# Kernel tuning notes

Measured on AMD Instinct MI355X. Metric: run time of the kernel, lower is better.

The kernel has to match this reference:

```python
import jax, jax.numpy as jnp
import numpy as np
from jax import lax

N, L, C_IN, NOISE_C, COMP, NC = 256, 512, 514, 112, 16, 2
MAIN_IN = NOISE_C + COMP  # 128
FEAT = NC * 4 * L         # 4096

def _conv1d(x, w, b, pad):
    # x [N,C,L], w [O,I,K]
    y = lax.conv_general_dilated(x, w, (1,), [(pad, pad)], dimension_numbers=('NCH', 'OIH', 'NCH'))
    return y + b[None, :, None]

def _bn(x, g, b):
    # BatchNorm1d, training mode: biased batch stats over (N, L)
    m = x.mean(axis=(0, 2), keepdims=True)
    v = x.var(axis=(0, 2), keepdims=True)
    return (x - m) * lax.rsqrt(v + 1e-5) * g[None, :, None] + b[None, :, None]

def _lrelu(x):
    return jnp.where(x >= 0, x, 0.2 * x)

def _pos_encode(length, dim):
    j = np.arange(dim)
    div = 1.0 / np.power(10000.0, 2 * (j[:, None] // 2) / dim)   # [dim,1]
    ang = np.arange(length)[None, :] * div                       # [dim,length]
    ang = np.where((j % 2 == 0)[:, None], np.sin(ang), np.cos(ang))
    return jnp.asarray(ang[None], jnp.float32)                   # [1,dim,length]

def _assemble(circle_prob, slider_prob):
    # Vectorized run-length label expansion equivalent to the per-sample python while-loop.
    # circle_prob [N, L/2, 2], slider_prob [N, L/4, 2] -> [N, L, 3]
    n, B = slider_prob.shape[0], slider_prob.shape[1]
    c = jnp.argmax(circle_prob, -1)
    s = jnp.argmax(slider_prob, -1)
    zc = jnp.zeros(circle_prob.shape[:-1] + (1,), circle_prob.dtype)
    zs = jnp.zeros(slider_prob.shape[:-1] + (1,), slider_prob.dtype)
    cp3 = jnp.concatenate([circle_prob, zc], -1)                                   # insert 0 at class 2
    sp3 = jnp.concatenate([slider_prob[..., :1], zs, slider_prob[..., 1:]], -1)    # insert 0 at class 1
    pad100 = jnp.array([1., 0., 0.], cp3.dtype)
    pad001 = jnp.array([0., 0., 1.], cp3.dtype)
    bidx = jnp.arange(B)[None, :]
    # slider-body blocks: slider run continues and not cut by sequence end
    body = (s == 1) & (bidx < B - 1)
    prev_body = jnp.concatenate([jnp.zeros((n, 1), bool), body[:, :-1]], 1)
    # tail block ends a slider run (either run stops, or boundary block)
    tail = ((s == 1) & (bidx == B - 1)) | ((s == 0) & prev_body)
    # circle emission for each half-step: prob row if predicted circle else pad
    cr0 = jnp.where((c == 1)[..., None], cp3, pad100).reshape(n, B, 2, 3)
    bodyE = body[..., None]
    row0 = jnp.where((body | tail)[..., None], sp3, cr0[:, :, 0, :])
    row1 = jnp.where(bodyE, pad001, pad100)
    row2 = jnp.where(bodyE, pad001, cr0[:, :, 1, :])
    row3 = jnp.where(bodyE, pad001, pad100)
    return jnp.stack([row0, row1, row2, row3], 2).reshape(n, 4 * B, 3)

def _forward(noise, cond_data, gumbel_u, ext_w1, ext_b1, ext_w2, ext_b2, ext_bn_g, ext_bn_b,
             m_w1, m_b1, m_w2, m_b2, m_bn_g, m_bn_b, lin_w, lin_b, circ_w, circ_b, slid_w, slid_b):
    # FeatureExtractor
    x = cond_data.transpose(0, 2, 1)                      # [N, 514, L]
    x = _lrelu(_conv1d(x, ext_w1, ext_b1, 0))             # [N, 32, L]
    cond = _bn(_conv1d(x, ext_w2, ext_b2, 1), ext_bn_g, ext_bn_b)  # [N, 16, L]
    gen_in = jnp.concatenate([cond, noise.transpose(0, 2, 1)], 1) + _pos_encode(L, MAIN_IN)  # [N,128,L]
    h = _lrelu(_conv1d(gen_in, m_w1, m_b1, 3))            # [N, 32, L]
    h = _lrelu(_bn(_conv1d(h, m_w2, m_b2, 1), m_bn_g, m_bn_b))     # [N, 8, L]
    flat = _lrelu(h.reshape(h.shape[0], -1) @ lin_w + lin_b)       # [N, 4096]
    circle_prob = (flat @ circ_w + circ_b).reshape(-1, L // 2, NC)
    slider_prob = (flat @ slid_w + slid_b).reshape(-1, L // 4, NC)
    out = _assemble(circle_prob, slider_prob)             # [N, L, 3]
    # gumbel_softmax(hard=True, tau=1)
    g = -jnp.log(-jnp.log(gumbel_u + 1e-10) + 1e-10)
    logits = out + g
    y_soft = jax.nn.softmax(logits, -1)
    y_hard = jax.nn.one_hot(jnp.argmax(logits, -1), 3, dtype=y_soft.dtype)
    gen_out = y_hard + y_soft - lax.stop_gradient(y_soft)
    return gen_out, cond

def setup_inputs() -> dict:
    key = jax.random.key(0)
    ks = jax.random.split(key, 12)
    def rn(k, shape, fan_in):
        return jax.random.normal(k, shape, jnp.float32) * (1.0 / fan_in) ** 0.5
    return {
        'noise': jax.random.normal(ks[0], (N, L, NOISE_C), jnp.float32),
        'cond_data': jax.random.normal(ks[1], (N, L, C_IN), jnp.float32),
        'gumbel_u': jax.random.uniform(ks[2], (N, L, 3), jnp.float32),
        'ext_w1': rn(ks[3], (C_IN // 16, C_IN, 1), C_IN), 'ext_b1': jnp.zeros(C_IN // 16),
        'ext_w2': rn(ks[4], (COMP, C_IN // 16, 3), 3 * (C_IN // 16)), 'ext_b2': jnp.zeros(COMP),
        'ext_bn_g': jnp.ones(COMP), 'ext_bn_b': jnp.zeros(COMP),
        'm_w1': rn(ks[5], (NC * 16, MAIN_IN, 7), 7 * MAIN_IN), 'm_b1': jnp.zeros(NC * 16),
        'm_w2': rn(ks[6], (NC * 4, NC * 16, 3), 3 * NC * 16), 'm_b2': jnp.zeros(NC * 4),
        'm_bn_g': jnp.ones(NC * 4), 'm_bn_b': jnp.zeros(NC * 4),
        'lin_w': rn(ks[7], (FEAT, FEAT), FEAT), 'lin_b': jnp.zeros(FEAT),
        'circ_w': rn(ks[8], (FEAT, NC * L // 2), FEAT), 'circ_b': jnp.zeros(NC * L // 2),
        'slid_w': rn(ks[9], (FEAT, NC * L // 4), FEAT), 'slid_b': jnp.zeros(NC * L // 4),
    }

def reference(noise, cond_data, gumbel_u, ext_w1, ext_b1, ext_w2, ext_b2, ext_bn_g, ext_bn_b,
              m_w1, m_b1, m_w2, m_b2, m_bn_g, m_bn_b, lin_w, lin_b, circ_w, circ_b, slid_w, slid_b):
    return _forward(noise, cond_data, gumbel_u, ext_w1, ext_b1, ext_w2, ext_b2, ext_bn_g, ext_bn_b,
                    m_w1, m_b1, m_w2, m_b2, m_bn_g, m_bn_b, lin_w, lin_b, circ_w, circ_b, slid_w, slid_b)
```

## Files before the change

### kernel.cpp

```cpp
#include <hip/hip_runtime.h>
#include <math.h>

#define NB 256
#define LL 512
#define CIN 514

__device__ __forceinline__ float lrelu(float x) { return x >= 0.f ? x : 0.2f * x; }

__global__ __launch_bounds__(256) void k_pos(float* __restrict__ pos) {
    int idx = blockIdx.x * 256 + threadIdx.x;
    int c = idx >> 9, l = idx & 511;
    double e = (double)(2 * (c >> 1)) / 128.0;
    double dv = 1.0 / pow(10000.0, e);
    double a = (double)l * dv;
    pos[idx] = (float)((c & 1) ? cos(a) : sin(a));
}

__global__ __launch_bounds__(256) void k_posconv(const float* __restrict__ POS, const float* __restrict__ W,
                                                 const float* __restrict__ bias, float* __restrict__ PC) {
    const int t = threadIdx.x;
    const int o = blockIdx.x >> 4, l0 = (blockIdx.x & 15) * 32;
    const int l = l0 + (t & 31), cs = t >> 5;
    float acc = 0.f;
    for (int ci = 0; ci < 16; ++ci) {
        int c = cs * 16 + ci;
        float wv[7];
#pragma unroll
        for (int k = 0; k < 7; ++k) wv[k] = W[o * 896 + c * 7 + k];
#pragma unroll
        for (int k = 0; k < 7; ++k) {
            int gl = l + k - 3;
            if (gl >= 0 && gl < LL) acc += wv[k] * POS[c * LL + gl];
        }
    }
    __shared__ float red[8][33];
    red[cs][t & 31] = acc;
    __syncthreads();
    if (cs == 0) {
        float s = bias[o];
#pragma unroll
        for (int j = 0; j < 8; ++j) s += red[j][t & 31];
        PC[o * LL + l0 + (t & 31)] = s;
    }
}

__global__ __launch_bounds__(256) void k_conv1(const float* __restrict__ X, const float* __restrict__ W,
                                               float* __restrict__ Pbase) {
    __shared__ __align__(16) float As[16][524];
    __shared__ __align__(16) float Bs[16][36];
    const int t = threadIdx.x;
    const int n = blockIdx.x >> 2, z = blockIdx.x & 3;
    const int kbase = z * 128;
    const int nch = (z == 3) ? 9 : 8;
    const int tl = t & 63, to = t >> 6;
    const size_t rowbase = (size_t)n * 512 * CIN;

    float acc[8][8];
#pragma unroll
    for (int oi = 0; oi < 8; ++oi)
#pragma unroll
        for (int p = 0; p < 8; ++p) acc[oi][p] = 0.f;

    float2 pf[16];
    float2 pfb;

    {
        const int kb = kbase;
#pragma unroll
        for (int ps = 0; ps < 16; ++ps) {
            int idx = ps * 256 + t;
            int pos = idx >> 3, kp = idx & 7;
            int gk = kb + kp * 2;
            float2 v = {0.f, 0.f};
            if (gk + 1 < CIN) v = *(const float2*)(X + rowbase + (size_t)pos * CIN + gk);
            else if (gk < CIN) v.x = X[rowbase + (size_t)pos * CIN + gk];
            pf[ps] = v;
        }
        {
            int o = t >> 3, kp = t & 7;
            int gk = kb + kp * 2;
            float2 v = {0.f, 0.f};
            if (gk + 1 < CIN) v = *(const float2*)(W + (size_t)o * CIN + gk);
            else if (gk < CIN) v.x = W[(size_t)o * CIN + gk];
            pfb = v;
        }
#pragma unroll
        for (int ps = 0; ps < 16; ++ps) {
            int idx = ps * 256 + t;
            int pos = idx >> 3, kp = idx & 7;
            As[kp * 2][pos] = pf[ps].x;
            As[kp * 2 + 1][pos] = pf[ps].y;
        }
        {
            int o = t >> 3, kp = t & 7;
            Bs[kp * 2][o] = pfb.x;
            Bs[kp * 2 + 1][o] = pfb.y;
        }
    }
    __syncthreads();

    for (int c = 0; c < nch; ++c) {
        if (c + 1 < nch) {
            const int kb = kbase + (c + 1) * 16;
#pragma unroll
            for (int ps = 0; ps < 16; ++ps) {
                int idx = ps * 256 + t;
                int pos = idx >> 3, kp = idx & 7;
                int gk = kb + kp * 2;
                float2 v = {0.f, 0.f};
                if (gk + 1 < CIN) v = *(const float2*)(X + rowbase + (size_t)pos * CIN + gk);
                else if (gk < CIN) v.x = X[rowbase + (size_t)pos * CIN + gk];
                pf[ps] = v;
            }
            int o = t >> 3, kp = t & 7;
            int gk = kb + kp * 2;
            float2 v = {0.f, 0.f};
            if (gk + 1 < CIN) v = *(const float2*)(W + (size_t)o * CIN + gk);
            else if (gk < CIN) v.x = W[(size_t)o * CIN + gk];
            pfb = v;
        }
#pragma unroll
        for (int kk = 0; kk < 16; ++kk) {
            float4 aL = *(const float4*)&As[kk][tl * 4];
            float4 aH = *(const float4*)&As[kk][256 + tl * 4];
            float4 b0 = *(const float4*)&Bs[kk][to * 8];
            float4 b1 = *(const float4*)&Bs[kk][to * 8 + 4];
            float av[8] = {aL.x, aL.y, aL.z, aL.w, aH.x, aH.y, aH.z, aH.w};
            float bv[8] = {b0.x, b0.y, b0.z, b0.w, b1.x, b1.y, b1.z, b1.w};
#pragma unroll
            for (int oi = 0; oi < 8; ++oi)
#pragma unroll
                for (int p = 0; p < 8; ++p) acc[oi][p] += av[p] * bv[oi];
        }
        __syncthreads();
        if (c + 1 < nch) {
#pragma unroll
            for (int ps = 0; ps < 16; ++ps) {
                int idx = ps * 256 + t;
                int pos = idx >> 3, kp = idx & 7;
                As[kp * 2][pos] = pf[ps].x;
                As[kp * 2 + 1][pos] = pf[ps].y;
            }
            int o = t >> 3, kp = t & 7;
            Bs[kp * 2][o] = pfb.x;
            Bs[kp * 2 + 1][o] = pfb.y;
        }
        __syncthreads();
    }

    float* P = Pbase + (size_t)z * 4194304;
#pragma unroll
    for (int oi = 0; oi < 8; ++oi) {
        int o = to * 8 + oi;
        float4 v0 = {acc[oi][0], acc[oi][1], acc[oi][2], acc[oi][3]};
        float4 v1 = {acc[oi][4], acc[oi][5], acc[oi][6], acc[oi][7]};
        *(float4*)(P + ((size_t)n * 32 + o) * LL + tl * 4) = v0;
        *(float4*)(P + ((size_t)n * 32 + o) * LL + 256 + tl * 4) = v1;
    }
}

__global__ __launch_bounds__(256) void k_conv2(const float* __restrict__ Pbase,
                                               const float* __restrict__ b1, const float* __restrict__ W,
                                               const float* __restrict__ bias, float* __restrict__ out) {
    __shared__ __align__(16) float Xs[32][264];
    __shared__ __align__(16) float Ws[16][32][4];
    const int t = threadIdx.x;
    const int n = blockIdx.x >> 1, l0 = (blockIdx.x & 1) * 256;
    for (int idx = t; idx < 32 * 258; idx += 256) {
        int i = idx / 258, j = idx % 258;
        int gl = l0 - 1 + j;
        float v = 0.f;
        if (gl >= 0 && gl < LL) {
            size_t off = ((size_t)n * 32 + i) * LL + gl;
            v = lrelu(Pbase[off] + Pbase[off + 4194304] + Pbase[off + 8388608] + Pbase[off + 12582912] + b1[i]);
        }
        Xs[i][j] = v;
    }
    for (int idx = t; idx < 1536; idx += 256) {
        int o = idx / 96, r = idx % 96;
        Ws[o][r / 3][r % 3] = W[idx];
    }
    __syncthreads();
    const int tx = t & 31, ty = t >> 5;
    float acc[2][8];
#pragma unroll
    for (int q = 0; q < 2; ++q)
#pragma unroll
        for (int p = 0; p < 8; ++p) acc[q][p] = 0.f;
    for (int i = 0; i < 32; ++i) {
        float4 a0 = *(const float4*)&Xs[i][tx*8];
        float4 a1 = *(const float4*)&Xs[i][tx*8+4];
        float4 a2 = *(const float4*)&Xs[i][tx*8+8];
        float a[12] = {a0.x,a0.y,a0.z,a0.w,a1.x,a1.y,a1.z,a1.w,a2.x,a2.y,a2.z,a2.w};
#pragma unroll
        for (int q = 0; q < 2; ++q) {
            float4 b = *(const float4*)&Ws[ty*2+q][i][0];
#pragma unroll
            for (int p = 0; p < 8; ++p)
                acc[q][p] += a[p]*b.x + a[p+1]*b.y + a[p+2]*b.z;
        }
    }
#pragma unroll
    for (int q = 0; q < 2; ++q) {
        int o = ty*2+q; float bb = bias[o];
#pragma unroll
        for (int h = 0; h < 2; ++h) {
            float4 v;
            v.x = acc[q][h*4+0] + bb; v.y = acc[q][h*4+1] + bb;
            v.z = acc[q][h*4+2] + bb; v.w = acc[q][h*4+3] + bb;
            *(float4*)(out + ((size_t)n*16 + o)*LL + l0 + tx*8 + h*4) = v;
        }
    }
}

__global__ __launch_bounds__(256) void k_redstats(const float* __restrict__ src, int C, float* __restrict__ part) {
    const int ch = blockIdx.x, sl = blockIdx.y, t = threadIdx.x;
    float s = 0.f, q = 0.f;
    for (int i = t; i < 4096; i += 256) {
        int n = sl*8 + (i >> 9), l = i & 511;
        float v = src[((size_t)n*C + ch)*LL + l];
        s += v; q += v*v;
    }
    __shared__ float rs[256], rq[256];
    rs[t] = s; rq[t] = q;
    __syncthreads();
    for (int off = 128; off > 0; off >>= 1) {
        if (t < off) { rs[t] += rs[t+off]; rq[t] += rq[t+off]; }
        __syncthreads();
    }
    if (t == 0) { part[(ch*32+sl)*2] = rs[0]; part[(ch*32+sl)*2+1] = rq[0]; }
}

__global__ void k_bnfinal(const float* __restrict__ part, const float* __restrict__ g,
                          const float* __restrict__ b, int C, float* __restrict__ ss) {
    int ch = threadIdx.x;
    if (ch >= C) return;
    float s = 0.f, q = 0.f;
    for (int j = 0; j < 32; ++j) { s += part[(ch*32 + j)*2]; q += part[(ch*32 + j)*2 + 1]; }
    float mean = s * (1.f/131072.f);
    float var = q * (1.f/131072.f) - mean*mean;
    float sc = g[ch] / sqrtf(var + 1e-5f);
    ss[ch] = sc;
    ss[C + ch] = b[ch] - mean * sc;
}

__global__ __launch_bounds__(256) void k_bnapply(const float* __restrict__ src, const float* __restrict__ ss,
        int C, float* __restrict__ dst, int act, int total4) {
    int i4 = blockIdx.x * 256 + threadIdx.x;
    if (i4 >= total4) return;
    int i = i4 << 2;
    int ch = (i >> 9) % C;
    float sc = ss[ch], sh = ss[C + ch];
    float4 v = reinterpret_cast<const float4*>(src)[i4];
    v.x = v.x*sc + sh; v.y = v.y*sc + sh; v.z = v.z*sc + sh; v.w = v.w*sc + sh;
    if (act) { v.x = lrelu(v.x); v.y = lrelu(v.y); v.z = lrelu(v.z); v.w = lrelu(v.w); }
    reinterpret_cast<float4*>(dst)[i4] = v;
}

__global__ __launch_bounds__(256) void k_mconv1(const float* __restrict__ C16, const float* __restrict__ NZ,
        const float* __restrict__ PC, const float* __restrict__ W,
        float* __restrict__ out0, float* __restrict__ out1) {
    __shared__ __align__(16) float Gs[2][8][268];
    __shared__ __align__(16) float Ws[2][32][8][8];
    const int t = threadIdx.x;
    const int n = blockIdx.x >> 2, l0 = ((blockIdx.x >> 1) & 1) * 256, z = blockIdx.x & 1;
    const int tx = t & 31, ty = t >> 5;
    float acc[4][8];
#pragma unroll
    for (int q = 0; q < 4; ++q)
#pragma unroll
        for (int p = 0; p < 8; ++p) acc[q][p] = 0.f;

    float4 ga0, ga1, gb0, gb1;
    float wpf[8];
    const int gl1 = l0 - 3 + t;
    const bool ok1 = (gl1 >= 0 && gl1 < LL);
    const int gl2 = l0 + 253 + t;
    const bool ok2 = (t < 6) && (gl2 < LL);

    auto LOADG = [&](int hh) {
        const float4 f4z = {0.f, 0.f, 0.f, 0.f};
        ga0 = f4z; ga1 = f4z; gb0 = f4z; gb1 = f4z;
        if (z == 0 && hh < 2) {
            const float* base = C16 + ((size_t)n * 16 + hh * 8) * LL;
            if (ok1) {
                const float* p = base + gl1;
                ga0.x = p[0];      ga0.y = p[LL];     ga0.z = p[2*LL];  ga0.w = p[3*LL];
                ga1.x = p[4*LL];   ga1.y = p[5*LL];   ga1.z = p[6*LL];  ga1.w = p[7*LL];
            }
            if (ok2) {
                const float* p = base + gl2;
                gb0.x = p[0];      gb0.y = p[LL];     gb0.z = p[2*LL];  gb0.w = p[3*LL];
                gb1.x = p[4*LL];   gb1.y = p[5*LL];   gb1.z = p[6*LL];  gb1.w = p[7*LL];
            }
        } else {
            const int nzc = z * 64 + hh * 8 - 16;
            if (ok1) {
                const float* p = NZ + ((size_t)n * LL + gl1) * 112 + nzc;
                ga0 = *(const float4*)p;
                ga1 = *(const float4*)(p + 4);
            }
            if (ok2) {
                const float* p = NZ + ((size_t)n * LL + gl2) * 112 + nzc;
                gb0 = *(const float4*)p;
                gb1 = *(const float4*)(p + 4);
            }
        }
    };
    auto WRITEG = [&](int bb) {
        Gs[bb][0][t] = ga0.x; Gs[bb][1][t] = ga0.y; Gs[bb][2][t] = ga0.z; Gs[bb][3][t] = ga0.w;
        Gs[bb][4][t] = ga1.x; Gs[bb][5][t] = ga1.y; Gs[bb][6][t] = ga1.z; Gs[bb][7][t] = ga1.w;
        if (t < 6) {
            Gs[bb][0][256+t] = gb0.x; Gs[bb][1][256+t] = gb0.y; Gs[bb][2][256+t] = gb0.z; Gs[bb][3][256+t] = gb0.w;
            Gs[bb][4][256+t] = gb1.x; Gs[bb][5][256+t] = gb1.y; Gs[bb][6][256+t] = gb1.z; Gs[bb][7][256+t] = gb1.w;
        }
    };
    auto LOADW = [&](int hh) {
        const int b7 = (z * 64 + hh * 8) * 7;
#pragma unroll
        for (int p = 0; p < 8; ++p) {
            int idx = p * 256 + t;
            int k = idx & 7, ci = (idx >> 3) & 7, o = idx >> 6;
            wpf[p] = (k < 7) ? W[(size_t)o * 896 + b7 + ci * 7 + k] : 0.f;
        }
    };
    auto WRITEW = [&](int bb) {
#pragma unroll
        for (int p = 0; p < 8; ++p) {
            int idx = p * 256 + t;
            int k = idx & 7;
            if (k < 7) {
                int ci = (idx >> 3) & 7, o = idx >> 6;
                Ws[bb][o][ci][k] = wpf[p];
            }
        }
    };

    LOADG(0);
    LOADW(0);
    WRITEG(0);
    WRITEW(0);
    __syncthreads();

    for (int h = 0; h < 8; ++h) {
        const int hb = h & 1;
        if (h < 7) {
            LOADG(h + 1);
            LOADW(h + 1);
        }
        for (int ci = 0; ci < 8; ++ci) {
            float4 a0 = *(const float4*)&Gs[hb][ci][tx*4];
            float4 a1 = *(const float4*)&Gs[hb][ci][tx*4+4];
            float4 a2 = *(const float4*)&Gs[hb][ci][tx*4+8];
            float4 a3 = *(const float4*)&Gs[hb][ci][128+tx*4];
            float4 a4 = *(const float4*)&Gs[hb][ci][128+tx*4+4];
            float4 a5 = *(const float4*)&Gs[hb][ci][128+tx*4+8];
            float aA[12] = {a0.x,a0.y,a0.z,a0.w,a1.x,a1.y,a1.z,a1.w,a2.x,a2.y,a2.z,a2.w};
            float aB[12] = {a3.x,a3.y,a3.z,a3.w,a4.x,a4.y,a4.z,a4.w,a5.x,a5.y,a5.z,a5.w};
#pragma unroll
            for (int q = 0; q < 4; ++q) {
                float4 b0 = *(const float4*)&Ws[hb][ty*4+q][ci][0];
                float4 b1 = *(const float4*)&Ws[hb][ty*4+q][ci][4];
                float b[7] = {b0.x,b0.y,b0.z,b0.w,b1.x,b1.y,b1.z};
#pragma unroll
                for (int p = 0; p < 4; ++p) {
#pragma unroll
                    for (int k = 0; k < 7; ++k) {
                        acc[q][p]   += aA[p+k]*b[k];
                        acc[q][4+p] += aB[p+k]*b[k];
                    }
                }
            }
        }
        if (h < 7) {
            const int nb = hb ^ 1;
            WRITEG(nb);
            WRITEW(nb);
            __syncthreads();
        }
    }

    float* out = z ? out1 : out0;
#pragma unroll
    for (int q = 0; q < 4; ++q) {
        int o = ty*4 + q;
        float4 p0 = {0.f,0.f,0.f,0.f}, p1 = {0.f,0.f,0.f,0.f};
        if (z == 0) {
            p0 = *(const float4*)(PC + o*LL + l0 + tx*4);
            p1 = *(const float4*)(PC + o*LL + l0 + 128 + tx*4);
        }
        float4 v0 = {acc[q][0]+p0.x, acc[q][1]+p0.y, acc[q][2]+p0.z, acc[q][3]+p0.w};
        float4 v1 = {acc[q][4]+p1.x, acc[q][5]+p1.y, acc[q][6]+p1.z, acc[q][7]+p1.w};
        *(float4*)(out + ((size_t)n*32 + o)*LL + l0 + tx*4) = v0;
        *(float4*)(out + ((size_t)n*32 + o)*LL + l0 + 128 + tx*4) = v1;
    }
}

__global__ __launch_bounds__(256) void k_mconv2(const float* __restrict__ P0, const float* __restrict__ P1,
        const float* __restrict__ W, const float* __restrict__ bias, float* __restrict__ out) {
    __shared__ __align__(16) float Xs[32][264];
    __shared__ __align__(16) float Ws[8][32][4];
    const int t = threadIdx.x;
    const int n = blockIdx.x >> 1, l0 = (blockIdx.x & 1) * 256;
    for (int idx = t; idx < 32 * 258; idx += 256) {
        int i = idx / 258, j = idx % 258;
        int gl = l0 - 1 + j;
        float v = 0.f;
        if (gl >= 0 && gl < LL) {
            size_t off = ((size_t)n * 32 + i) * LL + gl;
            v = lrelu(P0[off] + P1[off]);
        }
        Xs[i][j] = v;
    }
    for (int idx = t; idx < 768; idx += 256) {
        int o = idx / 96, r = idx % 96;
        Ws[o][r / 3][r % 3] = W[idx];
    }
    __syncthreads();
    const int tx = t & 31, ty = t >> 5;
    float acc[8];
#pragma unroll
    for (int p = 0; p < 8; ++p) acc[p] = 0.f;
    for (int i = 0; i < 32; ++i) {
        float4 a0 = *(const float4*)&Xs[i][tx*8];
        float4 a1 = *(const float4*)&Xs[i][tx*8+4];
        float4 a2 = *(const float4*)&Xs[i][tx*8+8];
        float a[12] = {a0.x,a0.y,a0.z,a0.w,a1.x,a1.y,a1.z,a1.w,a2.x,a2.y,a2.z,a2.w};
        float4 b = *(const float4*)&Ws[ty][i][0];
#pragma unroll
        for (int p = 0; p < 8; ++p)
            acc[p] += a[p]*b.x + a[p+1]*b.y + a[p+2]*b.z;
    }
    float bb = bias[ty];
#pragma unroll
    for (int h = 0; h < 2; ++h) {
        float4 v;
        v.x = acc[h*4+0] + bb; v.y = acc[h*4+1] + bb;
        v.z = acc[h*4+2] + bb; v.w = acc[h*4+3] + bb;
        *(float4*)(out + ((size_t)n*8 + ty)*LL + l0 + tx*8 + h*4) = v;
    }
}

__global__ __launch_bounds__(256) void k_lin(const float* __restrict__ A, const float* __restrict__ B,
                                             float* __restrict__ part) {
    __shared__ __align__(16) float As[16][132];
    __shared__ __align__(16) float Bs[16][132];
    const int t = threadIdx.x;
    const int bid = blockIdx.x;
    const int xcd = bid & 7, j = bid >> 3;
    const int z = j >> 3;
    const int m0 = ((j >> 2) & 1) * 128;
    const int f0 = (xcd * 4 + (j & 3)) * 128;
    const int k0base = z * 256;
    const int sar = t & 127, saq = t >> 7;
    const int sbr = t >> 4, sbq = t & 15;
    const int mq = (t & 15) * 4, fq = (t >> 4) * 4;

    float acc[8][8];
#pragma unroll
    for (int i = 0; i < 8; ++i)
#pragma unroll
        for (int q = 0; q < 8; ++q) acc[i][q] = 0.f;

    for (int it = 0; it < 16; ++it) {
        const int k0 = k0base + it * 16;
        {
            const float* pA = A + (size_t)(m0 + sar) * 4096 + k0 + saq * 8;
            float4 a0 = *(const float4*)(pA);
            float4 a1 = *(const float4*)(pA + 4);
            const float* pB = B + (size_t)(k0 + sbr) * 4096 + f0 + sbq * 8;
            float4 b0 = *(const float4*)(pB);
            float4 b1 = *(const float4*)(pB + 4);
            As[saq*8+0][sar] = a0.x; As[saq*8+1][sar] = a0.y; As[saq*8+2][sar] = a0.z; As[saq*8+3][sar] = a0.w;
            As[saq*8+4][sar] = a1.x; As[saq*8+5][sar] = a1.y; As[saq*8+6][sar] = a1.z; As[saq*8+7][sar] = a1.w;
            *(float4*)&Bs[sbr][sbq*8] = b0;
            *(float4*)&Bs[sbr][sbq*8+4] = b1;
        }
        __syncthreads();
#pragma unroll
        for (int kk = 0; kk < 16; ++kk) {
            float4 a0 = *(const float4*)&As[kk][mq];
            float4 a1 = *(const float4*)&As[kk][mq + 64];
            float4 b0 = *(const float4*)&Bs[kk][fq];
            float4 b1 = *(const float4*)&Bs[kk][fq + 64];
            float av[8] = {a0.x,a0.y,a0.z,a0.w,a1.x,a1.y,a1.z,a1.w};
            float bv[8] = {b0.x,b0.y,b0.z,b0.w,b1.x,b1.y,b1.z,b1.w};
#pragma unroll
            for (int i = 0; i < 8; ++i)
#pragma unroll
                for (int q = 0; q < 8; ++q) acc[i][q] += av[i] * bv[q];
        }
        __syncthreads();
    }

#pragma unroll
    for (int i = 0; i < 8; ++i) {
        int m = m0 + mq + (i & 3) + (i >> 2) * 64;
        float4 v0 = {acc[i][0], acc[i][1], acc[i][2], acc[i][3]};
        float4 v1 = {acc[i][4], acc[i][5], acc[i][6], acc[i][7]};
        *(float4*)(part + ((size_t)z * 256 + m) * 4096 + f0 + fq) = v0;
        *(float4*)(part + ((size_t)z * 256 + m) * 4096 + f0 + fq + 64) = v1;
    }
}

__global__ __launch_bounds__(256) void k_linred(const float* __restrict__ part, const float* __restrict__ bias,
        float* __restrict__ out) {
    int i4 = blockIdx.x*256 + threadIdx.x;
    int i = i4 << 2;
    int f = i & 4095;
    float4 s = *(const float4*)(bias + f);
#pragma unroll
    for (int zz = 0; zz < 16; ++zz) {
        float4 p = ((const float4*)(part + (size_t)zz * 1048576))[i4];
        s.x += p.x; s.y += p.y; s.z += p.z; s.w += p.w;
    }
    float4 r;
    r.x = lrelu(s.x); r.y = lrelu(s.y); r.z = lrelu(s.z); r.w = lrelu(s.w);
    ((float4*)out)[i4] = r;
}

__global__ __launch_bounds__(256) void k_heads(const float* __restrict__ A, const float* __restrict__ CW,
        const float* __restrict__ SW, float* __restrict__ part) {
    __shared__ __align__(16) float As[32][36];
    __shared__ __align__(16) float Bs[32][132];
    const int t = threadIdx.x;
    const int m0 = blockIdx.x * 32, f0 = blockIdx.y * 128, z = blockIdx.z;
    const float* B; int ldb, fb;
    if (f0 < 512) { B = CW; ldb = 512; fb = f0; } else { B = SW; ldb = 256; fb = f0 - 512; }
    const int tm = t & 7, tf = t >> 3;
    const int mi = t >> 3, kq = t & 7;
    float acc[4][4];
#pragma unroll
    for (int pm = 0; pm < 4; ++pm)
#pragma unroll
        for (int pf = 0; pf < 4; ++pf) acc[pm][pf] = 0.f;
    for (int k0 = z * 256; k0 < z * 256 + 256; k0 += 32) {
        float4 av = *(const float4*)(A + (size_t)(m0 + mi) * 4096 + k0 + kq * 4);
        As[kq*4+0][mi] = av.x; As[kq*4+1][mi] = av.y; As[kq*4+2][mi] = av.z; As[kq*4+3][mi] = av.w;
#pragma unroll
        for (int pass = 0; pass < 4; ++pass) {
            int fi = pass * 32 + kq * 4;
            *(float4*)&Bs[mi][fi] = *(const float4*)(B + (size_t)(k0 + mi) * ldb + fb + fi);
        }
        __syncthreads();
#pragma unroll 8
        for (int kk = 0; kk < 32; ++kk) {
            float4 a = *(const float4*)&As[kk][tm * 4];
            float4 b = *(const float4*)&Bs[kk][tf * 4];
            float avv[4] = {a.x,a.y,a.z,a.w};
            float bvv[4] = {b.x,b.y,b.z,b.w};
#pragma unroll
            for (int pm = 0; pm < 4; ++pm)
#pragma unroll
                for (int pf = 0; pf < 4; ++pf) acc[pm][pf] += avv[pm]*bvv[pf];
        }
        __syncthreads();
    }
#pragma unroll
    for (int pm = 0; pm < 4; ++pm) {
        float4 v = {acc[pm][0], acc[pm][1], acc[pm][2], acc[pm][3]};
        *(float4*)(part + ((size_t)z * 256 + m0 + tm * 4 + pm) * 768 + f0 + tf * 4) = v;
    }
}

__global__ __launch_bounds__(256) void k_assemble(const float* __restrict__ part, const float* __restrict__ cb,
        const float* __restrict__ sb, const float* __restrict__ gum, float* __restrict__ out) {
    __shared__ float buf[768];
    const int n = blockIdx.x;
    const int t = threadIdx.x;
#pragma unroll
    for (int rep = 0; rep < 3; ++rep) {
        int f = rep * 256 + t;
        float s = 0.f;
#pragma unroll
        for (int ks = 0; ks < 16; ++ks) s += part[((size_t)(ks * 256 + n)) * 768 + f];
        s += (f < 512) ? cb[f] : sb[f - 512];
        buf[f] = s;
    }
    __syncthreads();
    if (t >= 128) return;
    const int b = t;
    const float* cp = buf;
    const float* sp = buf + 512;
    float sl0 = sp[2*b], sl1 = sp[2*b+1];
    int s = sl1 > sl0 ? 1 : 0;
    int prevb = 0;
    if (b > 0) prevb = (sp[2*b-1] > sp[2*b-2]) ? 1 : 0;
    bool body = (s == 1) && (b < 127);
    bool tail = ((s == 1) && (b == 127)) || ((s == 0) && (prevb == 1));
    float c0a = cp[4*b], c0b = cp[4*b+1], c1a = cp[4*b+2], c1b = cp[4*b+3];
    bool cA = c0b > c0a, cB = c1b > c1a;
    float rows[4][3];
    if (body || tail)      { rows[0][0]=sl0; rows[0][1]=0.f; rows[0][2]=sl1; }
    else if (cA)           { rows[0][0]=c0a; rows[0][1]=c0b; rows[0][2]=0.f; }
    else                   { rows[0][0]=1.f; rows[0][1]=0.f; rows[0][2]=0.f; }
    if (body)              { rows[1][0]=0.f; rows[1][1]=0.f; rows[1][2]=1.f; }
    else                   { rows[1][0]=1.f; rows[1][1]=0.f; rows[1][2]=0.f; }
    if (body)              { rows[2][0]=0.f; rows[2][1]=0.f; rows[2][2]=1.f; }
    else if (cB)           { rows[2][0]=c1a; rows[2][1]=c1b; rows[2][2]=0.f; }
    else                   { rows[2][0]=1.f; rows[2][1]=0.f; rows[2][2]=0.f; }
    rows[3][0]=rows[1][0]; rows[3][1]=rows[1][1]; rows[3][2]=rows[1][2];
#pragma unroll
    for (int r = 0; r < 4; ++r) {
        int l = 4*b + r;
        const float* u = gum + ((size_t)n*512 + l)*3;
        float g0 = -logf(-logf(u[0]+1e-10f)+1e-10f);
        float g1 = -logf(-logf(u[1]+1e-10f)+1e-10f);
        float g2 = -logf(-logf(u[2]+1e-10f)+1e-10f);
        float t0 = rows[r][0]+g0, t1 = rows[r][1]+g1, t2 = rows[r][2]+g2;
        int am = 0; float mv = t0;
        if (t1 > mv) { am = 1; mv = t1; }
        if (t2 > mv) { am = 2; mv = t2; }
        float e0 = expf(t0-mv), e1 = expf(t1-mv), e2 = expf(t2-mv);
        float ssum = e0+e1+e2;
        float y0 = e0/ssum, y1 = e1/ssum, y2 = e2/ssum;
        float* o = out + ((size_t)n*512 + l)*3;
        o[0] = ((am==0?1.f:0.f) + y0) - y0;
        o[1] = ((am==1?1.f:0.f) + y1) - y1;
        o[2] = ((am==2?1.f:0.f) + y2) - y2;
    }
}

extern "C" void kernel_launch(void* const* d_in, const int* in_sizes, int n_in,
                              void* d_out, int out_size, void* d_ws, size_t ws_size,
                              hipStream_t stream) {
    const float* noise   = (const float*)d_in[0];
    const float* cond    = (const float*)d_in[1];
    const float* gumbel  = (const float*)d_in[2];
    const float* ext_w1  = (const float*)d_in[3];
    const float* ext_b1  = (const float*)d_in[4];
    const float* ext_w2  = (const float*)d_in[5];
    const float* ext_b2  = (const float*)d_in[6];
    const float* ext_bng = (const float*)d_in[7];
    const float* ext_bnb = (const float*)d_in[8];
    const float* m_w1    = (const float*)d_in[9];
    const float* m_b1    = (const float*)d_in[10];
    const float* m_w2    = (const float*)d_in[11];
    const float* m_b2    = (const float*)d_in[12];
    const float* m_bng   = (const float*)d_in[13];
    const float* m_bnb   = (const float*)d_in[14];
    const float* lin_w   = (const float*)d_in[15];
    const float* lin_b   = (const float*)d_in[16];
    const float* circ_w  = (const float*)d_in[17];
    const float* circ_b  = (const float*)d_in[18];
    const float* slid_w  = (const float*)d_in[19];
    const float* slid_b  = (const float*)d_in[20];

    float* genout  = (float*)d_out;
    float* condout = (float*)d_out + 256*512*3;

    float* w     = (float*)d_ws;
    float* ws0   = w;
    float* y2    = ws0 + 16777216;
    float* posb  = y2 + 2097152;
    float* pc    = posb + 65536;
    float* flatB = pc + 16384;
    float* partH = flatB + 1048576;
    float* stats = partH + 3145728;

    k_pos<<<256, 256, 0, stream>>>(posb);
    k_posconv<<<512, 256, 0, stream>>>(posb, m_w1, m_b1, pc);
    k_conv1<<<1024, 256, 0, stream>>>(cond, ext_w1, ws0);
    k_conv2<<<512, 256, 0, stream>>>(ws0, ext_b1, ext_w2, ext_b2, y2);
    k_redstats<<<dim3(16,32), 256, 0, stream>>>(y2, 16, stats);
    k_bnfinal<<<1, 64, 0, stream>>>(stats, ext_bng, ext_bnb, 16, stats + 2048);
    k_bnapply<<<2048, 256, 0, stream>>>(y2, stats + 2048, 16, condout, 0, 524288);
    k_mconv1<<<1024, 256, 0, stream>>>(condout, noise, pc, m_w1, ws0, ws0 + 4194304);
    k_mconv2<<<512, 256, 0, stream>>>(ws0, ws0 + 4194304, m_w2, m_b2, y2);
    k_redstats<<<dim3(8,32), 256, 0, stream>>>(y2, 8, stats);
    k_bnfinal<<<1, 64, 0, stream>>>(stats, m_bng, m_bnb, 8, stats + 2048 + 64);
    k_bnapply<<<1024, 256, 0, stream>>>(y2, stats + 2048 + 64, 8, y2, 1, 262144);
    k_lin<<<1024, 256, 0, stream>>>(y2, lin_w, ws0);
    k_linred<<<1024, 256, 0, stream>>>(ws0, lin_b, flatB);
    k_heads<<<dim3(8,6,16), 256, 0, stream>>>(flatB, circ_w, slid_w, partH);
    k_assemble<<<256, 256, 0, stream>>>(partH, circ_b, slid_b, gumbel, genout);
}
```

Baseline: 526.9 us.

## Fuse BN stat reduction into conv epilogues and register-prefetch GEMM tiles

Removes the separate k_redstats passes by computing per-block sum and sum-of-squares in the k_conv2 and k_mconv2 epilogues and writing 512 partials per channel, which k_bnfinal now reduces. The k_lin and k_heads loops now load the next K tile into registers while the current shared-memory tile is being consumed, so global load latency can overlap with the FMAs. The cost is an extra barrier per iteration, more register pressure in the GEMMs, and a longer serial loop in the single-block bnfinal kernel.

```diff
diff --git a/kernel.cpp b/kernel.cpp
--- a/kernel.cpp
+++ b/kernel.cpp
@@ -161,11 +161,14 @@
 
 __global__ __launch_bounds__(256) void k_conv2(const float* __restrict__ Pbase,
                                                const float* __restrict__ b1, const float* __restrict__ W,
-                                               const float* __restrict__ bias, float* __restrict__ out) {
+                                               const float* __restrict__ bias, float* __restrict__ out,
+                                               float* __restrict__ part) {
     __shared__ __align__(16) float Xs[32][264];
     __shared__ __align__(16) float Ws[16][32][4];
+    __shared__ float reds[16][33], redq[16][33];
     const int t = threadIdx.x;
-    const int n = blockIdx.x >> 1, l0 = (blockIdx.x & 1) * 256;
+    const int bid = blockIdx.x;
+    const int n = bid >> 1, l0 = (bid & 1) * 256;
     for (int idx = t; idx < 32 * 258; idx += 256) {
         int i = idx / 258, j = idx % 258;
         int gl = l0 - 1 + j;
@@ -203,40 +206,35 @@
 #pragma unroll
     for (int q = 0; q < 2; ++q) {
         int o = ty*2+q; float bb = bias[o];
+        float s = 0.f, sq = 0.f;
 #pragma unroll
         for (int h = 0; h < 2; ++h) {
             float4 v;
             v.x = acc[q][h*4+0] + bb; v.y = acc[q][h*4+1] + bb;
             v.z = acc[q][h*4+2] + bb; v.w = acc[q][h*4+3] + bb;
+            s += v.x + v.y + v.z + v.w;
+            sq += v.x*v.x + v.y*v.y + v.z*v.z + v.w*v.w;
             *(float4*)(out + ((size_t)n*16 + o)*LL + l0 + tx*8 + h*4) = v;
         }
-    }
-}
-
-__global__ __launch_bounds__(256) void k_redstats(const float* __restrict__ src, int C, float* __restrict__ part) {
-    const int ch = blockIdx.x, sl = blockIdx.y, t = threadIdx.x;
-    float s = 0.f, q = 0.f;
-    for (int i = t; i < 4096; i += 256) {
-        int n = sl*8 + (i >> 9), l = i & 511;
-        float v = src[((size_t)n*C + ch)*LL + l];
-        s += v; q += v*v;
-    }
-    __shared__ float rs[256], rq[256];
-    rs[t] = s; rq[t] = q;
-    __syncthreads();
-    for (int off = 128; off > 0; off >>= 1) {
-        if (t < off) { rs[t] += rs[t+off]; rq[t] += rq[t+off]; }
-        __syncthreads();
-    }
-    if (t == 0) { part[(ch*32+sl)*2] = rs[0]; part[(ch*32+sl)*2+1] = rq[0]; }
+        reds[o][tx] = s;
+        redq[o][tx] = sq;
+    }
+    __syncthreads();
+    if (t < 16) {
+        float s = 0.f, sq = 0.f;
+#pragma unroll
+        for (int x = 0; x < 32; ++x) { s += reds[t][x]; sq += redq[t][x]; }
+        part[((size_t)t * 512 + bid) * 2] = s;
+        part[((size_t)t * 512 + bid) * 2 + 1] = sq;
+    }
 }
 
 __global__ void k_bnfinal(const float* __restrict__ part, const float* __restrict__ g,
-                          const float* __restrict__ b, int C, float* __restrict__ ss) {
+                          const float* __restrict__ b, int C, int S, float* __restrict__ ss) {
     int ch = threadIdx.x;
     if (ch >= C) return;
     float s = 0.f, q = 0.f;
-    for (int j = 0; j < 32; ++j) { s += part[(ch*32 + j)*2]; q += part[(ch*32 + j)*2 + 1]; }
+    for (int j = 0; j < S; ++j) { s += part[((size_t)ch*S + j)*2]; q += part[((size_t)ch*S + j)*2 + 1]; }
     float mean = s * (1.f/131072.f);
     float var = q * (1.f/131072.f) - mean*mean;
     float sc = g[ch] / sqrtf(var + 1e-5f);
@@ -397,11 +395,14 @@
 }
 
 __global__ __launch_bounds__(256) void k_mconv2(const float* __restrict__ P0, const float* __restrict__ P1,
-        const float* __restrict__ W, const float* __restrict__ bias, float* __restrict__ out) {
+        const float* __restrict__ W, const float* __restrict__ bias, float* __restrict__ out,
+        float* __restrict__ part) {
     __shared__ __align__(16) float Xs[32][264];
     __shared__ __align__(16) float Ws[8][32][4];
+    __shared__ float reds[8][33], redq[8][33];
     const int t = threadIdx.x;
-    const int n = blockIdx.x >> 1, l0 = (blockIdx.x & 1) * 256;
+    const int bid = blockIdx.x;
+    const int n = bid >> 1, l0 = (bid & 1) * 256;
     for (int idx = t; idx < 32 * 258; idx += 256) {
         int i = idx / 258, j = idx % 258;
         int gl = l0 - 1 + j;
@@ -432,12 +433,25 @@
             acc[p] += a[p]*b.x + a[p+1]*b.y + a[p+2]*b.z;
     }
     float bb = bias[ty];
+    float s = 0.f, sq = 0.f;
 #pragma unroll
     for (int h = 0; h < 2; ++h) {
         float4 v;
         v.x = acc[h*4+0] + bb; v.y = acc[h*4+1] + bb;
         v.z = acc[h*4+2] + bb; v.w = acc[h*4+3] + bb;
+        s += v.x + v.y + v.z + v.w;
+        sq += v.x*v.x + v.y*v.y + v.z*v.z + v.w*v.w;
         *(float4*)(out + ((size_t)n*8 + ty)*LL + l0 + tx*8 + h*4) = v;
+    }
+    reds[ty][tx] = s;
+    redq[ty][tx] = sq;
+    __syncthreads();
+    if (t < 8) {
+        float ss = 0.f, qq = 0.f;
+#pragma unroll
+        for (int x = 0; x < 32; ++x) { ss += reds[t][x]; qq += redq[t][x]; }
+        part[((size_t)t * 512 + bid) * 2] = ss;
+        part[((size_t)t * 512 + bid) * 2 + 1] = qq;
     }
 }
 
@@ -462,21 +476,32 @@
 #pragma unroll
         for (int q = 0; q < 8; ++q) acc[i][q] = 0.f;
 
+    float4 pa0, pa1, pb0, pb1;
+    {
+        const int k0 = k0base;
+        const float* pA = A + (size_t)(m0 + sar) * 4096 + k0 + saq * 8;
+        pa0 = *(const float4*)(pA);
+        pa1 = *(const float4*)(pA + 4);
+        const float* pB = B + (size_t)(k0 + sbr) * 4096 + f0 + sbq * 8;
+        pb0 = *(const float4*)(pB);
+        pb1 = *(const float4*)(pB + 4);
+        As[saq*8+0][sar] = pa0.x; As[saq*8+1][sar] = pa0.y; As[saq*8+2][sar] = pa0.z; As[saq*8+3][sar] = pa0.w;
+        As[saq*8+4][sar] = pa1.x; As[saq*8+5][sar] = pa1.y; As[saq*8+6][sar] = pa1.z; As[saq*8+7][sar] = pa1.w;
+        *(float4*)&Bs[sbr][sbq*8] = pb0;
+        *(float4*)&Bs[sbr][sbq*8+4] = pb1;
+    }
+    __syncthreads();
+
     for (int it = 0; it < 16; ++it) {
-        const int k0 = k0base + it * 16;
-        {
+        if (it + 1 < 16) {
+            const int k0 = k0base + (it + 1) * 16;
             const float* pA = A + (size_t)(m0 + sar) * 4096 + k0 + saq * 8;
-            float4 a0 = *(const float4*)(pA);
-            float4 a1 = *(const float4*)(pA + 4);
+            pa0 = *(const float4*)(pA);
+            pa1 = *(const float4*)(pA + 4);
             const float* pB = B + (size_t)(k0 + sbr) * 4096 + f0 + sbq * 8;
-            float4 b0 = *(const float4*)(pB);
-            float4 b1 = *(const float4*)(pB + 4);
-            As[saq*8+0][sar] = a0.x; As[saq*8+1][sar] = a0.y; As[saq*8+2][sar] = a0.z; As[saq*8+3][sar] = a0.w;
-            As[saq*8+4][sar] = a1.x; As[saq*8+5][sar] = a1.y; As[saq*8+6][sar] = a1.z; As[saq*8+7][sar] = a1.w;
-            *(float4*)&Bs[sbr][sbq*8] = b0;
-            *(float4*)&Bs[sbr][sbq*8+4] = b1;
-        }
-        __syncthreads();
+            pb0 = *(const float4*)(pB);
+            pb1 = *(const float4*)(pB + 4);
+        }
 #pragma unroll
         for (int kk = 0; kk < 16; ++kk) {
             float4 a0 = *(const float4*)&As[kk][mq];
@@ -489,6 +514,13 @@
             for (int i = 0; i < 8; ++i)
 #pragma unroll
                 for (int q = 0; q < 8; ++q) acc[i][q] += av[i] * bv[q];
+        }
+        __syncthreads();
+        if (it + 1 < 16) {
+            As[saq*8+0][sar] = pa0.x; As[saq*8+1][sar] = pa0.y; As[saq*8+2][sar] = pa0.z; As[saq*8+3][sar] = pa0.w;
+            As[saq*8+4][sar] = pa1.x; As[saq*8+5][sar] = pa1.y; As[saq*8+6][sar] = pa1.z; As[saq*8+7][sar] = pa1.w;
+            *(float4*)&Bs[sbr][sbq*8] = pb0;
+            *(float4*)&Bs[sbr][sbq*8+4] = pb1;
         }
         __syncthreads();
     }
@@ -534,15 +566,29 @@
     for (int pm = 0; pm < 4; ++pm)
 #pragma unroll
         for (int pf = 0; pf < 4; ++pf) acc[pm][pf] = 0.f;
-    for (int k0 = z * 256; k0 < z * 256 + 256; k0 += 32) {
-        float4 av = *(const float4*)(A + (size_t)(m0 + mi) * 4096 + k0 + kq * 4);
-        As[kq*4+0][mi] = av.x; As[kq*4+1][mi] = av.y; As[kq*4+2][mi] = av.z; As[kq*4+3][mi] = av.w;
-#pragma unroll
-        for (int pass = 0; pass < 4; ++pass) {
-            int fi = pass * 32 + kq * 4;
-            *(float4*)&Bs[mi][fi] = *(const float4*)(B + (size_t)(k0 + mi) * ldb + fb + fi);
-        }
-        __syncthreads();
+
+    float4 pav, pbv[4];
+    {
+        const int k0 = z * 256;
+        pav = *(const float4*)(A + (size_t)(m0 + mi) * 4096 + k0 + kq * 4);
+#pragma unroll
+        for (int pass = 0; pass < 4; ++pass)
+            pbv[pass] = *(const float4*)(B + (size_t)(k0 + mi) * ldb + fb + pass * 32 + kq * 4);
+        As[kq*4+0][mi] = pav.x; As[kq*4+1][mi] = pav.y; As[kq*4+2][mi] = pav.z; As[kq*4+3][mi] = pav.w;
+#pragma unroll
+        for (int pass = 0; pass < 4; ++pass)
+            *(float4*)&Bs[mi][pass * 32 + kq * 4] = pbv[pass];
+    }
+    __syncthreads();
+
+    for (int it = 0; it < 8; ++it) {
+        if (it + 1 < 8) {
+            const int k0 = z * 256 + (it + 1) * 32;
+            pav = *(const float4*)(A + (size_t)(m0 + mi) * 4096 + k0 + kq * 4);
+#pragma unroll
+            for (int pass = 0; pass < 4; ++pass)
+                pbv[pass] = *(const float4*)(B + (size_t)(k0 + mi) * ldb + fb + pass * 32 + kq * 4);
+        }
 #pragma unroll 8
         for (int kk = 0; kk < 32; ++kk) {
             float4 a = *(const float4*)&As[kk][tm * 4];
@@ -553,6 +599,13 @@
             for (int pm = 0; pm < 4; ++pm)
 #pragma unroll
                 for (int pf = 0; pf < 4; ++pf) acc[pm][pf] += avv[pm]*bvv[pf];
+        }
+        __syncthreads();
+        if (it + 1 < 8) {
+            As[kq*4+0][mi] = pav.x; As[kq*4+1][mi] = pav.y; As[kq*4+2][mi] = pav.z; As[kq*4+3][mi] = pav.w;
+#pragma unroll
+            for (int pass = 0; pass < 4; ++pass)
+                *(float4*)&Bs[mi][pass * 32 + kq * 4] = pbv[pass];
         }
         __syncthreads();
     }
@@ -656,20 +709,21 @@
     float* pc    = posb + 65536;
     float* flatB = pc + 16384;
     float* partH = flatB + 1048576;
-    float* stats = partH + 3145728;
+    float* statA = partH + 3145728;
+    float* ssA   = statA + 16384;
+    float* statB = ssA + 64;
+    float* ssB   = statB + 8192;
 
     k_pos<<<256, 256, 0, stream>>>(posb);
     k_posconv<<<512, 256, 0, stream>>>(posb, m_w1, m_b1, pc);
     k_conv1<<<1024, 256, 0, stream>>>(cond, ext_w1, ws0);
-    k_conv2<<<512, 256, 0, stream>>>(ws0, ext_b1, ext_w2, ext_b2, y2);
-    k_redstats<<<dim3(16,32), 256, 0, stream>>>(y2, 16, stats);
-    k_bnfinal<<<1, 64, 0, stream>>>(stats, ext_bng, ext_bnb, 16, stats + 2048);
-    k_bnapply<<<2048, 256, 0, stream>>>(y2, stats + 2048, 16, condout, 0, 524288);
+    k_conv2<<<512, 256, 0, stream>>>(ws0, ext_b1, ext_w2, ext_b2, y2, statA);
+    k_bnfinal<<<1, 64, 0, stream>>>(statA, ext_bng, ext_bnb, 16, 512, ssA);
+    k_bnapply<<<2048, 256, 0, stream>>>(y2, ssA, 16, condout, 0, 524288);
     k_mconv1<<<1024, 256, 0, stream>>>(condout, noise, pc, m_w1, ws0, ws0 + 4194304);
-    k_mconv2<<<512, 256, 0, stream>>>(ws0, ws0 + 4194304, m_w2, m_b2, y2);
-    k_redstats<<<dim3(8,32), 256, 0, stream>>>(y2, 8, stats);
-    k_bnfinal<<<1, 64, 0, stream>>>(stats, m_bng, m_bnb, 8, stats + 2048 + 64);
-    k_bnapply<<<1024, 256, 0, stream>>>(y2, stats + 2048 + 64, 8, y2, 1, 262144);
+    k_mconv2<<<512, 256, 0, stream>>>(ws0, ws0 + 4194304, m_w2, m_b2, y2, statB);
+    k_bnfinal<<<1, 64, 0, stream>>>(statB, m_bng, m_bnb, 8, 512, ssB);
+    k_bnapply<<<1024, 256, 0, stream>>>(y2, ssB, 8, y2, 1, 262144);
     k_lin<<<1024, 256, 0, stream>>>(y2, lin_w, ws0);
     k_linred<<<1024, 256, 0, stream>>>(ws0, lin_b, flatB);
     k_heads<<<dim3(8,6,16), 256, 0, stream>>>(flatB, circ_w, slid_w, partH);
```

After: 638.7 us. 1.21x slower.
